# Kernel tuning notes

Hardware: AMD Instinct MI355X
Metric: run time of the kernel (lower is better)

## Reference

```python
import jax, jax.numpy as jnp
import numpy as np

C = 64          # n_channels
NCLS = 10       # output_size
EPS = 1e-5      # GroupNorm eps (torch default)
T0, DT, NSTEPS = 0.0, 0.1, 10  # t0=0, t1=1, dt=0.1 -> 10 fixed RK4 steps


def _gn(x, w, b):
    # GroupNorm(C, C): per-sample, per-channel norm over H,W
    m = x.mean(axis=(2, 3), keepdims=True)
    v = ((x - m) ** 2).mean(axis=(2, 3), keepdims=True)
    return (x - m) * jax.lax.rsqrt(v + EPS) * w[None, :, None, None] + b[None, :, None, None]


def _conv(x, w, b, stride, pad):
    y = jax.lax.conv_general_dilated(x, w, (stride, stride), pad,
                                     dimension_numbers=('NCHW', 'OIHW', 'NCHW'))
    return y + b[None, :, None, None]


def setup_inputs() -> dict:
    key = jax.random.key(0)
    ks = jax.random.split(key, 8)
    rnd = lambda k, shape, s: jax.random.normal(k, shape, jnp.float32) * s
    B = 64
    return dict(
        x=jax.random.normal(ks[0], (B, 1, 130, 130), jnp.float32),
        # downsampler: Conv(1->C,3,1,VALID), GN, ReLU, Conv(C->C,4,2,1), GN, ReLU, Conv(C->C,4,2,1)
        ds_w1=rnd(ks[1], (C, 1, 3, 3), 0.2), ds_b1=jnp.zeros((C,), jnp.float32),
        ds_n1w=jnp.ones((C,), jnp.float32), ds_n1b=jnp.zeros((C,), jnp.float32),
        ds_w2=rnd(ks[2], (C, C, 4, 4), 0.03), ds_b2=jnp.zeros((C,), jnp.float32),
        ds_n2w=jnp.ones((C,), jnp.float32), ds_n2b=jnp.zeros((C,), jnp.float32),
        ds_w3=rnd(ks[3], (C, C, 4, 4), 0.03), ds_b3=jnp.zeros((C,), jnp.float32),
        # ODE RHS: two Conv2d(C+1 -> C, 3, 1, 1) with time channel concat, two GroupNorms
        ode_w1=rnd(ks[4], (C, C + 1, 3, 3), 0.04), ode_b1=jnp.zeros((C,), jnp.float32),
        ode_n1w=jnp.ones((C,), jnp.float32), ode_n1b=jnp.zeros((C,), jnp.float32),
        ode_w2=rnd(ks[5], (C, C + 1, 3, 3), 0.04), ode_b2=jnp.zeros((C,), jnp.float32),
        ode_n2w=jnp.ones((C,), jnp.float32), ode_n2b=jnp.zeros((C,), jnp.float32),
        # classification head: GN, ReLU, GAP, Linear(C -> 10)
        head_nw=jnp.ones((C,), jnp.float32), head_nb=jnp.zeros((C,), jnp.float32),
        head_W=rnd(ks[6], (NCLS, C), 0.1), head_b=jnp.zeros((NCLS,), jnp.float32),
    )


def reference(x, ds_w1, ds_b1, ds_n1w, ds_n1b, ds_w2, ds_b2, ds_n2w, ds_n2b, ds_w3, ds_b3,
              ode_w1, ode_b1, ode_n1w, ode_n1b, ode_w2, ode_b2, ode_n2w, ode_n2b,
              head_nw, head_nb, head_W, head_b):
    P1 = [(1, 1), (1, 1)]
    # ---- downsampler ----
    h = _conv(x, ds_w1, ds_b1, 1, 'VALID')                      # [B,C,128,128]
    h = jax.nn.relu(_gn(h, ds_n1w, ds_n1b))
    h = _conv(h, ds_w2, ds_b2, 2, P1)                           # [B,C,64,64]
    h = jax.nn.relu(_gn(h, ds_n2w, ds_n2b))
    h = _conv(h, ds_w3, ds_b3, 2, P1)                           # [B,C,32,32]

    # ---- ODE layer: fixed-step classic RK4 (tableau_low), 10 steps ----
    def rhs(t, z):
        z = jax.nn.relu(_gn(z, ode_n1w, ode_n1b))
        ts = jnp.full_like(z[:, :1], t)
        z = _conv(jnp.concatenate((ts, z), axis=1), ode_w1, ode_b1, 1, P1)
        z = jax.nn.relu(_gn(z, ode_n2w, ode_n2b))
        ts = jnp.full_like(z[:, :1], t)
        z = _conv(jnp.concatenate((ts, z), axis=1), ode_w2, ode_b2, 1, P1)
        return z

    def step(z, i):
        t = T0 + i * DT
        k1 = rhs(t, z)
        k2 = rhs(t + 0.5 * DT, z + 0.5 * DT * k1)
        k3 = rhs(t + 0.5 * DT, z + 0.5 * DT * k2)
        k4 = rhs(t + DT, z + DT * k3)
        return z + (DT / 6.0) * (k1 + 2.0 * k2 + 2.0 * k3 + k4), None

    h, _ = jax.lax.scan(step, h, jnp.arange(NSTEPS, dtype=jnp.float32))

    # ---- classification head ----
    h = jax.nn.relu(_gn(h, head_nw, head_nb))
    h = h.mean(axis=(2, 3))                                     # AdaptiveAvgPool2d((1,1)) + Flatten
    return h @ head_W.T + head_b                                # [B, 10]
```

## Files before the change

kernel.cpp:

```cpp
#include <hip/hip_runtime.h>

#define BB 64
#define CC 64

typedef __attribute__((ext_vector_type(8))) short short8;
typedef __attribute__((ext_vector_type(4))) short short4v;
typedef __attribute__((ext_vector_type(4))) float f32x4;

__device__ __forceinline__ float bf2f(unsigned short h) {
    unsigned int u = ((unsigned int)h) << 16;
    float f; __builtin_memcpy(&f, &u, 4); return f;
}
__device__ __forceinline__ unsigned short f2bf(float f) {
    unsigned int u; __builtin_memcpy(&u, &f, 4);
    u += 0x7fffu + ((u >> 16) & 1u);
    return (unsigned short)(u >> 16);
}

__global__ __launch_bounds__(256) void conv1stats_kernel(const float* __restrict__ x,
    const float* __restrict__ w1, const float* __restrict__ b1,
    float* __restrict__ ps, float* __restrict__ ps2) {
    __shared__ float sw1[576];
    __shared__ float sb1[64];
    __shared__ float xs[10 * 130];
    int tid = threadIdx.x;
    int qq = blockIdx.x;
    int b = blockIdx.y;
    for (int i = tid; i < 576; i += 256) sw1[i] = w1[i];
    if (tid < 64) sb1[tid] = b1[tid];
    const float* xb = x + (size_t)b * 130 * 130;
    int c = tid >> 2, q = tid & 3;
    float s = 0.f, s2 = 0.f;
    for (int sidx = 0; sidx < 2; sidx++) {
        int row0 = (qq * 2 + sidx) * 8;
        __syncthreads();
        for (int i = tid; i < 1300; i += 256) xs[i] = xb[row0 * 130 + i];
        __syncthreads();
        const float* wc = &sw1[c * 9];
        float bc = sb1[c];
        for (int p = q; p < 1024; p += 4) {
            int y = p >> 7, xx = p & 127;
            float v = bc;
#pragma unroll
            for (int ky = 0; ky < 3; ky++)
#pragma unroll
                for (int kx = 0; kx < 3; kx++)
                    v += xs[(y + ky) * 130 + xx + kx] * wc[ky * 3 + kx];
            s += v; s2 += v * v;
        }
    }
    s  += __shfl_xor(s, 1, 64);  s  += __shfl_xor(s, 2, 64);
    s2 += __shfl_xor(s2, 1, 64); s2 += __shfl_xor(s2, 2, 64);
    if (q == 0) {
        ps [(b * 8 + qq) * 64 + c] = s;
        ps2[(b * 8 + qq) * 64 + c] = s2;
    }
}

__global__ __launch_bounds__(256) void gn1fin_kernel(const float* __restrict__ ps,
    const float* __restrict__ ps2, const float* __restrict__ n1w, const float* __restrict__ n1b,
    float* __restrict__ gn1sc, float* __restrict__ gn1sh) {
    int i = blockIdx.x * 256 + threadIdx.x;
    if (i >= BB * CC) return;
    int c = i & 63, b = i >> 6;
    float s = 0.f, s2 = 0.f;
#pragma unroll
    for (int qq = 0; qq < 8; qq++) {
        s  += ps [(b * 8 + qq) * 64 + c];
        s2 += ps2[(b * 8 + qq) * 64 + c];
    }
    float mean = s / 16384.f;
    float var = s2 / 16384.f - mean * mean;
    float rstd = rsqrtf(var + 1e-5f);
    float sc = rstd * n1w[c];
    gn1sc[i] = sc;
    gn1sh[i] = n1b[c] - mean * sc;
}

__global__ __launch_bounds__(256) void prepack_kernel(const float* __restrict__ w1,
    const float* __restrict__ w2, const float* __restrict__ dw2,
    const float* __restrict__ dw3, unsigned short* __restrict__ Apk,
    float* __restrict__ Stab) {
    int set = blockIdx.y, kc = blockIdx.x, tid = threadIdx.x;
    int nchunk = (set < 2) ? 18 : 32;
    if (kc < nchunk) {
        const float* w = (set == 0) ? w1 : (set == 1) ? w2 : (set == 2) ? dw2 : dw3;
        size_t off = (set == 0) ? 0 : (set == 1) ? 36864 : (set == 2) ? 73728 : 139264;
        for (int e = tid; e < 2048; e += 256) {
            int co = e >> 5, j = e & 31;
            int k = kc * 32 + j;
            int ci = k & 63;
            int tap = k >> 6;
            float val;
            if (set < 2) val = w[(co * 65 + ci + 1) * 9 + tap];
            else         val = w[((co << 6) + ci) * 16 + tap];
            Apk[off + (size_t)kc * 2048 + e] = f2bf(val);
        }
    }
    if (set < 2 && kc == 0) {
        const float* w = set ? w2 : w1;
        for (int t = tid; t < 576; t += 256) {
            int co = t / 9, tap = t % 9;
            Stab[set * 576 + t] = w[(co * 65) * 9 + tap];
        }
    }
}

__global__ __launch_bounds__(256) void ds2mfma_kernel(const float* __restrict__ x,
    const float* __restrict__ w1, const float* __restrict__ b1,
    const float* __restrict__ gn1sc, const float* __restrict__ gn1sh,
    const unsigned short* __restrict__ Apk, const float* __restrict__ bias2,
    unsigned short* __restrict__ h2, float* __restrict__ sums_out) {
    __shared__ unsigned short X[2 * 198 * 64];
    __shared__ float xs[8 * 68];
    __shared__ float sw1[576];
    __shared__ float sb1[64], ssc[64], ssh[64], sb2[64];
    __shared__ float sred[4][64], s2red[4][64];
    int tid = threadIdx.x;
    int b = blockIdx.y;
    int bx = blockIdx.x;
    int xh = bx & 1, sy = bx >> 1;
    int lane = tid & 63, w = tid >> 6;
    int colL = lane & 15, quad = lane >> 4;

    for (int i = tid; i < 576; i += 256) sw1[i] = w1[i];
    if (tid < 64) {
        sb1[tid] = b1[tid];
        ssc[tid] = gn1sc[b * 64 + tid];
        ssh[tid] = gn1sh[b * 64 + tid];
        sb2[tid] = bias2[tid];
    }
    {
        const float* xb = x + (size_t)b * 130 * 130;
        for (int i = tid; i < 544; i += 256) {
            int r = i / 68, cc = i % 68;
            int xr = 4 * sy - 1 + r, xcg = 64 * xh - 1 + cc;
            xs[i] = (xr >= 0 && xr < 130 && xcg >= 0 && xcg < 130) ? xb[xr * 130 + xcg] : 0.f;
        }
    }
    __syncthreads();
    {
        int sub = tid & 7;
        float sbr[8], scr[8], shr[8];
#pragma unroll
        for (int e = 0; e < 8; e++) {
            int c = sub * 8 + e;
            sbr[e] = sb1[c]; scr[e] = ssc[c]; shr[e] = ssh[c];
        }
        for (int i = tid; i < 3168; i += 256) {
            int pidx = i >> 3;
            int ir = pidx / 66, ic = pidx - ir * 66;
            int gy = 4 * sy - 1 + ir, gxg = 64 * xh - 1 + ic;
            short8 o;
            if (gy >= 0 && gy < 128 && gxg >= 0 && gxg < 128) {
#pragma unroll
                for (int e = 0; e < 8; e++) {
                    int c = sub * 8 + e;
                    float v = sbr[e];
#pragma unroll
                    for (int ky = 0; ky < 3; ky++)
#pragma unroll
                        for (int kx = 0; kx < 3; kx++)
                            v += xs[(ir + ky) * 68 + ic + kx] * sw1[c * 9 + ky * 3 + kx];
                    o[e] = (short)f2bf(fmaxf(fmaf(v, scr[e], shr[e]), 0.f));
                }
            } else {
#pragma unroll
                for (int e = 0; e < 8; e++) o[e] = 0;
            }
            int p = ic & 1;
            int psx = ir * 33 + (ic >> 1);
            *(short8*)(X + ((p * 198 + psx) << 6) + ((sub ^ (psx & 7)) << 3)) = o;
        }
    }
    __syncthreads();

    int l = w >> 1, oxb = (w & 1) * 16;
    int oxl = oxb + colL;
    f32x4 acc[4] = {};
    for (int kc = 0; kc < 32; ++kc) {
        int tap = kc >> 1;
        int ky = tap >> 2, kx = tap & 3;
        int chgrp = (kc & 1) * 4 + quad;
        int ir = 2 * l + ky;
        int p = kx & 1;
        int psx = ir * 33 + oxl + (kx >> 1);
        short8 bb = *(const short8*)(X + ((p * 198 + psx) << 6) + ((chgrp ^ (psx & 7)) << 3));
        const unsigned short* ap = Apk + (((kc << 6) + colL) << 5) + (quad << 3);
        short8 a0 = *(const short8*)(ap);
        short8 a1 = *(const short8*)(ap + 512);
        short8 a2 = *(const short8*)(ap + 1024);
        short8 a3 = *(const short8*)(ap + 1536);
        acc[0] = __builtin_amdgcn_mfma_f32_16x16x32_bf16(a0, bb, acc[0], 0, 0, 0);
        acc[1] = __builtin_amdgcn_mfma_f32_16x16x32_bf16(a1, bb, acc[1], 0, 0, 0);
        acc[2] = __builtin_amdgcn_mfma_f32_16x16x32_bf16(a2, bb, acc[2], 0, 0, 0);
        acc[3] = __builtin_amdgcn_mfma_f32_16x16x32_bf16(a3, bb, acc[3], 0, 0, 0);
    }

    float sl[16], s2l[16];
#pragma unroll
    for (int i = 0; i < 16; i++) { sl[i] = 0.f; s2l[i] = 0.f; }
    int oy = 2 * sy + l, oxg = xh * 32 + oxl;
#pragma unroll
    for (int mt = 0; mt < 4; ++mt) {
        int co0 = mt * 16 + quad * 4;
        size_t base = ((size_t)((b * 64 + oy) * 64 + oxg)) * 64 + co0;
        short4v o;
#pragma unroll
        for (int r = 0; r < 4; ++r) {
            unsigned short hh = f2bf(acc[mt][r] + sb2[co0 + r]);
            o[r] = (short)hh;
            float f = bf2f(hh);
            sl[mt * 4 + r] += f; s2l[mt * 4 + r] += f * f;
        }
        *(short4v*)(h2 + base) = o;
    }
#pragma unroll
    for (int idx = 0; idx < 16; ++idx) {
        float s = sl[idx], s2 = s2l[idx];
        s += __shfl_xor(s, 1, 64); s += __shfl_xor(s, 2, 64);
        s += __shfl_xor(s, 4, 64); s += __shfl_xor(s, 8, 64);
        s2 += __shfl_xor(s2, 1, 64); s2 += __shfl_xor(s2, 2, 64);
        s2 += __shfl_xor(s2, 4, 64); s2 += __shfl_xor(s2, 8, 64);
        if (colL == 0) {
            int co = (idx >> 2) * 16 + quad * 4 + (idx & 3);
            sred[w][co] = s; s2red[w][co] = s2;
        }
    }
    __syncthreads();
    if (tid < 64) {
        float s = sred[0][tid] + sred[1][tid] + sred[2][tid] + sred[3][tid];
        float s2 = s2red[0][tid] + s2red[1][tid] + s2red[2][tid] + s2red[3][tid];
        atomicAdd(&sums_out[b * 64 + tid], s);
        atomicAdd(&sums_out[4096 + b * 64 + tid], s2);
    }
}

__global__ __launch_bounds__(256) void ds3mfma_kernel(const unsigned short* __restrict__ h2,
    const float* __restrict__ sums_in, const float* __restrict__ gw, const float* __restrict__ gb,
    const unsigned short* __restrict__ Apk, const float* __restrict__ bias3,
    float* __restrict__ z, unsigned short* __restrict__ zb, float* __restrict__ sums_out) {
    __shared__ unsigned short X[2 * 198 * 64];
    __shared__ float ssc[64], ssh[64], sb3[64];
    __shared__ float sred[4][64], s2red[4][64];
    int tid = threadIdx.x;
    int b = blockIdx.y, sy = blockIdx.x;
    int lane = tid & 63, w = tid >> 6;
    int colL = lane & 15, quad = lane >> 4;

    if (tid < 64) {
        int c = tid;
        float s = sums_in[b * 64 + c];
        float s2 = sums_in[4096 + b * 64 + c];
        float mean = s * (1.f / 4096.f);
        float var = fmaxf(s2 * (1.f / 4096.f) - mean * mean, 0.f);
        float sc = rsqrtf(var + 1e-5f) * gw[c];
        ssc[c] = sc;
        ssh[c] = gb[c] - mean * sc;
        sb3[c] = bias3[c];
    }
    __syncthreads();
    {
        int sub = tid & 7;
        float scr[8], shr[8];
#pragma unroll
        for (int e = 0; e < 8; e++) { scr[e] = ssc[sub * 8 + e]; shr[e] = ssh[sub * 8 + e]; }
        for (int i = tid; i < 3168; i += 256) {
            int pidx = i >> 3;
            int ir = pidx / 66, ic = pidx - ir * 66;
            int gy = 4 * sy - 1 + ir, gx = ic - 1;
            short8 o;
            if (gy >= 0 && gy < 64 && gx >= 0 && gx < 64) {
                short8 d = *(const short8*)(h2 + ((size_t)((b * 64 + gy) * 64 + gx)) * 64 + sub * 8);
#pragma unroll
                for (int e = 0; e < 8; e++) {
                    float f = bf2f((unsigned short)d[e]);
                    o[e] = (short)f2bf(fmaxf(fmaf(f, scr[e], shr[e]), 0.f));
                }
            } else {
#pragma unroll
                for (int e = 0; e < 8; e++) o[e] = 0;
            }
            int p = ic & 1;
            int psx = ir * 33 + (ic >> 1);
            *(short8*)(X + ((p * 198 + psx) << 6) + ((sub ^ (psx & 7)) << 3)) = o;
        }
    }
    __syncthreads();

    int l = w >> 1, oxb = (w & 1) * 16;
    int oxl = oxb + colL;
    f32x4 acc[4] = {};
    for (int kc = 0; kc < 32; ++kc) {
        int tap = kc >> 1;
        int ky = tap >> 2, kx = tap & 3;
        int chgrp = (kc & 1) * 4 + quad;
        int ir = 2 * l + ky;
        int p = kx & 1;
        int psx = ir * 33 + oxl + (kx >> 1);
        short8 bb = *(const short8*)(X + ((p * 198 + psx) << 6) + ((chgrp ^ (psx & 7)) << 3));
        const unsigned short* ap = Apk + (((kc << 6) + colL) << 5) + (quad << 3);
        short8 a0 = *(const short8*)(ap);
        short8 a1 = *(const short8*)(ap + 512);
        short8 a2 = *(const short8*)(ap + 1024);
        short8 a3 = *(const short8*)(ap + 1536);
        acc[0] = __builtin_amdgcn_mfma_f32_16x16x32_bf16(a0, bb, acc[0], 0, 0, 0);
        acc[1] = __builtin_amdgcn_mfma_f32_16x16x32_bf16(a1, bb, acc[1], 0, 0, 0);
        acc[2] = __builtin_amdgcn_mfma_f32_16x16x32_bf16(a2, bb, acc[2], 0, 0, 0);
        acc[3] = __builtin_amdgcn_mfma_f32_16x16x32_bf16(a3, bb, acc[3], 0, 0, 0);
    }

    float sl[16], s2l[16];
#pragma unroll
    for (int i = 0; i < 16; i++) { sl[i] = 0.f; s2l[i] = 0.f; }
    int py = 2 * sy + l;
#pragma unroll
    for (int mt = 0; mt < 4; ++mt) {
        int co0 = mt * 16 + quad * 4;
        size_t base = ((size_t)((b << 10) + py * 32 + oxl)) * 64 + co0;
        f32x4 zv;
        short4v o;
#pragma unroll
        for (int r = 0; r < 4; ++r) {
            float val = acc[mt][r] + sb3[co0 + r];
            zv[r] = val;
            unsigned short hh = f2bf(val);
            o[r] = (short)hh;
            float f = bf2f(hh);
            sl[mt * 4 + r] += f; s2l[mt * 4 + r] += f * f;
        }
        *(f32x4*)(z + base) = zv;
        *(short4v*)(zb + base) = o;
    }
#pragma unroll
    for (int idx = 0; idx < 16; ++idx) {
        float s = sl[idx], s2 = s2l[idx];
        s += __shfl_xor(s, 1, 64); s += __shfl_xor(s, 2, 64);
        s += __shfl_xor(s, 4, 64); s += __shfl_xor(s, 8, 64);
        s2 += __shfl_xor(s2, 1, 64); s2 += __shfl_xor(s2, 2, 64);
        s2 += __shfl_xor(s2, 4, 64); s2 += __shfl_xor(s2, 8, 64);
        if (colL == 0) {
            int co = (idx >> 2) * 16 + quad * 4 + (idx & 3);
            sred[w][co] = s; s2red[w][co] = s2;
        }
    }
    __syncthreads();
    if (tid < 64) {
        float s = sred[0][tid] + sred[1][tid] + sred[2][tid] + sred[3][tid];
        float s2 = s2red[0][tid] + s2red[1][tid] + s2red[2][tid] + s2red[3][tid];
        atomicAdd(&sums_out[b * 64 + tid], s);
        atomicAdd(&sums_out[4096 + b * 64 + tid], s2);
    }
}

#define CONV_LDS_BYTES 124416
__global__ __launch_bounds__(512, 2) void convmfma_kernel(
    const unsigned short* __restrict__ uin, const float* __restrict__ sums_in,
    const float* __restrict__ gw, const float* __restrict__ gb,
    const unsigned short* __restrict__ Apk, const float* __restrict__ stab,
    const float* __restrict__ bias, float t, float aa, int mode,
    float* __restrict__ z, unsigned short* __restrict__ uout,
    float* __restrict__ kacc, float* __restrict__ sums_out)
{
    extern __shared__ unsigned short smem[];
    unsigned short* Aw = smem;
    unsigned short* X  = smem + 36864;
    float* fp    = (float*)(smem + 36864 + 21760);
    float* ssc   = fp;        float* ssh   = fp + 64;
    float* tS    = fp + 128;  float* trow0 = fp + 192;  float* trow2 = fp + 256;
    float* tcol0 = fp + 320;  float* tcol2 = fp + 384;
    float* tc00  = fp + 448;  float* tc02  = fp + 512;
    float* tc20  = fp + 576;  float* tc22  = fp + 640;
    float* sred  = fp + 704;
    float* s2red = fp + 1216;

    int tid = threadIdx.x;
    int b = blockIdx.y, strip = blockIdx.x;
    int y0 = strip * 8;
    int lane = tid & 63, w = tid >> 6;
    int colL = lane & 15, quad = lane >> 4;

    {
        f32x4 zz = 0.f;
        for (int i = tid; i < 2720; i += 512) ((f32x4*)X)[i] = zz;
    }
    for (int i = tid; i < 4608; i += 512) ((f32x4*)Aw)[i] = ((const f32x4*)Apk)[i];

    if (tid < 64) {
        int c = tid;
        float s = sums_in[b * 64 + c];
        float s2 = sums_in[4096 + b * 64 + c];
        float mean = s * (1.f / 1024.f);
        float var = fmaxf(s2 * (1.f / 1024.f) - mean * mean, 0.f);
        float sc = rsqrtf(var + 1e-5f) * gw[c];
        ssc[c] = sc;
        ssh[c] = gb[c] - mean * sc;
    } else if (tid < 128) {
        int co = tid - 64;
        float w0[9];
#pragma unroll
        for (int k = 0; k < 9; k++) w0[k] = stab[co * 9 + k] * t;
        tS[co] = bias[co] + w0[0]+w0[1]+w0[2]+w0[3]+w0[4]+w0[5]+w0[6]+w0[7]+w0[8];
        trow0[co] = w0[0] + w0[1] + w0[2];
        trow2[co] = w0[6] + w0[7] + w0[8];
        tcol0[co] = w0[0] + w0[3] + w0[6];
        tcol2[co] = w0[2] + w0[5] + w0[8];
        tc00[co] = w0[0]; tc02[co] = w0[2]; tc20[co] = w0[6]; tc22[co] = w0[8];
    }
    __syncthreads();

    {
        int sub = tid & 7;
        float scr[8], shr[8];
#pragma unroll
        for (int e = 0; e < 8; e++) { scr[e] = ssc[sub * 8 + e]; shr[e] = ssh[sub * 8 + e]; }
#pragma unroll
        for (int it = 0; it < 5; ++it) {
            int pidx = (tid >> 3) + it * 64;
            int r = pidx >> 5, xc = pidx & 31;
            int gy = y0 - 1 + r;
            if (gy < 0 || gy > 31) continue;
            int gp = (b << 10) + gy * 32 + xc;
            short8 d = *(const short8*)(uin + (size_t)gp * 64 + sub * 8);
            short8 o;
#pragma unroll
            for (int e = 0; e < 8; e++) {
                float f = bf2f((unsigned short)d[e]);
                o[e] = (short)f2bf(fmaxf(fmaf(f, scr[e], shr[e]), 0.f));
            }
            int psx = r * 34 + xc + 1;
            *(short8*)(X + (psx << 6) + ((sub ^ (psx & 7)) << 3)) = o;
        }
    }
    __syncthreads();

    f32x4 acc[4][2] = {};
    for (int kc = 0; kc < 18; ++kc) {
        int tap = kc >> 1;
        int dy = tap / 3, dx = tap % 3;
        int chgrp = (kc & 1) * 4 + quad;
        int ps0 = (w + dy) * 34 + colL + dx;
        int ps1 = ps0 + 16;
        short8 bb0 = *(const short8*)(X + (ps0 << 6) + ((chgrp ^ (ps0 & 7)) << 3));
        short8 bb1 = *(const short8*)(X + (ps1 << 6) + ((chgrp ^ (ps1 & 7)) << 3));
        const unsigned short* ap = Aw + (((kc << 6) + colL) << 5) + (quad << 3);
        short8 a0 = *(const short8*)(ap);
        short8 a1 = *(const short8*)(ap + 512);
        short8 a2 = *(const short8*)(ap + 1024);
        short8 a3 = *(const short8*)(ap + 1536);
        acc[0][0] = __builtin_amdgcn_mfma_f32_16x16x32_bf16(a0, bb0, acc[0][0], 0, 0, 0);
        acc[0][1] = __builtin_amdgcn_mfma_f32_16x16x32_bf16(a0, bb1, acc[0][1], 0, 0, 0);
        acc[1][0] = __builtin_amdgcn_mfma_f32_16x16x32_bf16(a1, bb0, acc[1][0], 0, 0, 0);
        acc[1][1] = __builtin_amdgcn_mfma_f32_16x16x32_bf16(a1, bb1, acc[1][1], 0, 0, 0);
        acc[2][0] = __builtin_amdgcn_mfma_f32_16x16x32_bf16(a2, bb0, acc[2][0], 0, 0, 0);
        acc[2][1] = __builtin_amdgcn_mfma_f32_16x16x32_bf16(a2, bb1, acc[2][1], 0, 0, 0);
        acc[3][0] = __builtin_amdgcn_mfma_f32_16x16x32_bf16(a3, bb0, acc[3][0], 0, 0, 0);
        acc[3][1] = __builtin_amdgcn_mfma_f32_16x16x32_bf16(a3, bb1, acc[3][1], 0, 0, 0);
    }

    float sl[16], s2l[16];
#pragma unroll
    for (int i = 0; i < 16; i++) { sl[i] = 0.f; s2l[i] = 0.f; }
    int py = y0 + w;
    bool by0 = (py == 0), by1 = (py == 31);
#pragma unroll
    for (int nt = 0; nt < 2; ++nt) {
        int px = nt * 16 + colL;
        bool bx0 = (px == 0), bx1 = (px == 31);
#pragma unroll
        for (int mt = 0; mt < 4; ++mt) {
            int co0 = mt * 16 + quad * 4;
            float vout[4];
#pragma unroll
            for (int r = 0; r < 4; ++r) {
                int co = co0 + r;
                float val = acc[mt][nt][r] + tS[co];
                if (by0) { val -= trow0[co]; if (bx0) val += tc00[co]; if (bx1) val += tc02[co]; }
                if (by1) { val -= trow2[co]; if (bx0) val += tc20[co]; if (bx1) val += tc22[co]; }
                if (bx0) val -= tcol0[co];
                if (bx1) val -= tcol2[co];
                vout[r] = val;
            }
            size_t base = ((size_t)((b << 10) + py * 32 + px)) * 64 + co0;
            if (mode == 3) {
                short4v o;
#pragma unroll
                for (int r = 0; r < 4; ++r) {
                    unsigned short hh = f2bf(vout[r]);
                    o[r] = (short)hh;
                    float f = bf2f(hh);
                    sl[mt * 4 + r] += f; s2l[mt * 4 + r] += f * f;
                }
                *(short4v*)(uout + base) = o;
            } else if (mode == 2) {
                f32x4 kv = *(const f32x4*)(kacc + base);
                f32x4 zv = *(const f32x4*)(z + base);
                short4v o;
#pragma unroll
                for (int r = 0; r < 4; ++r) {
                    float zn = zv[r] + aa * (kv[r] + vout[r]);
                    zv[r] = zn;
                    unsigned short hh = f2bf(zn);
                    o[r] = (short)hh;
                    float f = bf2f(hh);
                    sl[mt * 4 + r] += f; s2l[mt * 4 + r] += f * f;
                }
                *(f32x4*)(z + base) = zv;
                *(short4v*)(uout + base) = o;
            } else {
                f32x4 zv = *(const f32x4*)(z + base);
                f32x4 kv;
                if (mode == 1) {
                    kv = *(const f32x4*)(kacc + base);
#pragma unroll
                    for (int r = 0; r < 4; ++r) kv[r] += 2.f * vout[r];
                } else {
#pragma unroll
                    for (int r = 0; r < 4; ++r) kv[r] = vout[r];
                }
                *(f32x4*)(kacc + base) = kv;
                short4v o;
#pragma unroll
                for (int r = 0; r < 4; ++r) {
                    unsigned short hh = f2bf(zv[r] + aa * vout[r]);
                    o[r] = (short)hh;
                    float f = bf2f(hh);
                    sl[mt * 4 + r] += f; s2l[mt * 4 + r] += f * f;
                }
                *(short4v*)(uout + base) = o;
            }
        }
    }
#pragma unroll
    for (int idx = 0; idx < 16; ++idx) {
        float s = sl[idx], s2 = s2l[idx];
        s += __shfl_xor(s, 1, 64); s += __shfl_xor(s, 2, 64);
        s += __shfl_xor(s, 4, 64); s += __shfl_xor(s, 8, 64);
        s2 += __shfl_xor(s2, 1, 64); s2 += __shfl_xor(s2, 2, 64);
        s2 += __shfl_xor(s2, 4, 64); s2 += __shfl_xor(s2, 8, 64);
        if (colL == 0) {
            int co = (idx >> 2) * 16 + quad * 4 + (idx & 3);
            sred[w * 64 + co] = s; s2red[w * 64 + co] = s2;
        }
    }
    __syncthreads();
    if (tid < 64) {
        float s = 0.f, s2 = 0.f;
#pragma unroll
        for (int i = 0; i < 8; i++) { s += sred[i * 64 + tid]; s2 += s2red[i * 64 + tid]; }
        atomicAdd(&sums_out[b * 64 + tid], s);
        atomicAdd(&sums_out[4096 + b * 64 + tid], s2);
    }
}

__global__ __launch_bounds__(256) void headgap_kernel(const float* __restrict__ z,
    const float* __restrict__ w, const float* __restrict__ b, float* __restrict__ pooled) {
    __shared__ float r1[4][64], r2[4][64];
    __shared__ float scs[64], shs[64];
    int bq = blockIdx.x, tid = threadIdx.x;
    int c = tid & 63, g = tid >> 6;
    float s = 0.f, s2 = 0.f;
    for (int p = g; p < 1024; p += 4) {
        float v = z[((size_t)((bq << 10) + p)) * 64 + c];
        s += v; s2 += v * v;
    }
    r1[g][c] = s; r2[g][c] = s2;
    __syncthreads();
    if (tid < 64) {
        float ts = r1[0][tid] + r1[1][tid] + r1[2][tid] + r1[3][tid];
        float ts2 = r2[0][tid] + r2[1][tid] + r2[2][tid] + r2[3][tid];
        float mean = ts / 1024.f;
        float var = fmaxf(ts2 / 1024.f - mean * mean, 0.f);
        float sc = rsqrtf(var + 1e-5f) * w[tid];
        scs[tid] = sc;
        shs[tid] = b[tid] - mean * sc;
    }
    __syncthreads();
    float sc = scs[c], sh = shs[c];
    float r = 0.f;
    for (int p = g; p < 1024; p += 4)
        r += fmaxf(fmaf(z[((size_t)((bq << 10) + p)) * 64 + c], sc, sh), 0.f);
    r1[g][c] = r;
    __syncthreads();
    if (tid < 64)
        pooled[bq * 64 + tid] = (r1[0][tid] + r1[1][tid] + r1[2][tid] + r1[3][tid]) / 1024.f;
}

__global__ __launch_bounds__(256) void headfc_kernel(const float* __restrict__ pooled,
    const float* __restrict__ W, const float* __restrict__ bias, float* __restrict__ out) {
    int i = blockIdx.x * 256 + threadIdx.x;
    if (i < 640) {
        int b = i / 10, j = i % 10;
        float a = bias[j];
        const float* p = pooled + b * 64;
        const float* wj = W + j * 64;
#pragma unroll 8
        for (int c = 0; c < 64; c++) a += p[c] * wj[c];
        out[i] = a;
    }
}

extern "C" void kernel_launch(void* const* d_in, const int* in_sizes, int n_in,
                              void* d_out, int out_size, void* d_ws, size_t ws_size,
                              hipStream_t stream) {
    const float* x      = (const float*)d_in[0];
    const float* ds_w1  = (const float*)d_in[1];
    const float* ds_b1  = (const float*)d_in[2];
    const float* ds_n1w = (const float*)d_in[3];
    const float* ds_n1b = (const float*)d_in[4];
    const float* ds_w2  = (const float*)d_in[5];
    const float* ds_b2  = (const float*)d_in[6];
    const float* ds_n2w = (const float*)d_in[7];
    const float* ds_n2b = (const float*)d_in[8];
    const float* ds_w3  = (const float*)d_in[9];
    const float* ds_b3  = (const float*)d_in[10];
    const float* ode_w1 = (const float*)d_in[11];
    const float* ode_b1 = (const float*)d_in[12];
    const float* ode_n1w= (const float*)d_in[13];
    const float* ode_n1b= (const float*)d_in[14];
    const float* ode_w2 = (const float*)d_in[15];
    const float* ode_b2 = (const float*)d_in[16];
    const float* ode_n2w= (const float*)d_in[17];
    const float* ode_n2b= (const float*)d_in[18];
    const float* head_nw= (const float*)d_in[19];
    const float* head_nb= (const float*)d_in[20];
    const float* head_W = (const float*)d_in[21];
    const float* head_b = (const float*)d_in[22];

    const size_t NZ = (size_t)BB * CC * 32 * 32;
    float* ws = (float*)d_ws;
    float*          z     = ws;
    unsigned short* zb    = (unsigned short*)(ws + NZ);
    unsigned short* u     = (unsigned short*)(ws + 3 * NZ / 2);
    unsigned short* v     = (unsigned short*)(ws + 2 * NZ);
    float*          kacc  = ws + 5 * NZ / 2;
    unsigned short* h2    = u;
    float*          apf   = ws + 7 * NZ / 2;
    unsigned short* Apk   = (unsigned short*)apf;
    float*          Stab  = apf + 102400;
    float*          sums  = Stab + 1152;
    float*          ps    = sums + 82 * 8192;
    float*          ps2   = ps + 32768;
    float*          gn1sc = ps2 + 32768;
    float*          gn1sh = gn1sc + 4096;
    float*          pooled= gn1sh + 4096;

    auto SUM = [&](int s) { return sums + (size_t)s * 8192; };
    auto SV = [&](int i, int j) { return 1 + i * 7 + j; };
    auto SU = [&](int i, int j) { return 1 + i * 7 + 4 + j; };
    auto ZS = [&](int i) { return 71 + i; };
    const int H2S = 81;

    hipFuncSetAttribute(reinterpret_cast<const void*>(convmfma_kernel),
                        hipFuncAttributeMaxDynamicSharedMemorySize, CONV_LDS_BYTES);

    hipMemsetAsync(sums, 0, 82 * 8192 * sizeof(float), stream);
    prepack_kernel<<<dim3(32, 4), 256, 0, stream>>>(ode_w1, ode_w2, ds_w2, ds_w3, Apk, Stab);

    conv1stats_kernel<<<dim3(8, BB), 256, 0, stream>>>(x, ds_w1, ds_b1, ps, ps2);
    gn1fin_kernel<<<16, 256, 0, stream>>>(ps, ps2, ds_n1w, ds_n1b, gn1sc, gn1sh);
    ds2mfma_kernel<<<dim3(64, BB), 256, 0, stream>>>(x, ds_w1, ds_b1, gn1sc, gn1sh,
        Apk + 73728, ds_b2, h2, SUM(H2S));
    ds3mfma_kernel<<<dim3(16, BB), 256, 0, stream>>>(h2, SUM(H2S), ds_n2w, ds_n2b,
        Apk + 139264, ds_b3, z, zb, SUM(0));

    const unsigned short* AP1 = Apk;
    const unsigned short* AP2 = Apk + 36864;
    const float* ST1 = Stab;
    const float* ST2 = Stab + 576;
    const float c6 = 0.1f / 6.0f;
    dim3 cgrid(4, BB);
    for (int i = 0; i < 10; i++) {
        float t0 = 0.1f * (float)i;
        int zslot = (i == 0) ? 0 : ZS(i - 1);
        convmfma_kernel<<<cgrid, 512, CONV_LDS_BYTES, stream>>>(zb, SUM(zslot), ode_n1w, ode_n1b,
            AP1, ST1, ode_b1, t0, 0.f, 3, z, v, kacc, SUM(SV(i, 0)));
        convmfma_kernel<<<cgrid, 512, CONV_LDS_BYTES, stream>>>(v, SUM(SV(i, 0)), ode_n2w, ode_n2b,
            AP2, ST2, ode_b2, t0, 0.05f, 0, z, u, kacc, SUM(SU(i, 0)));
        convmfma_kernel<<<cgrid, 512, CONV_LDS_BYTES, stream>>>(u, SUM(SU(i, 0)), ode_n1w, ode_n1b,
            AP1, ST1, ode_b1, t0 + 0.05f, 0.f, 3, z, v, kacc, SUM(SV(i, 1)));
        convmfma_kernel<<<cgrid, 512, CONV_LDS_BYTES, stream>>>(v, SUM(SV(i, 1)), ode_n2w, ode_n2b,
            AP2, ST2, ode_b2, t0 + 0.05f, 0.05f, 1, z, u, kacc, SUM(SU(i, 1)));
        convmfma_kernel<<<cgrid, 512, CONV_LDS_BYTES, stream>>>(u, SUM(SU(i, 1)), ode_n1w, ode_n1b,
            AP1, ST1, ode_b1, t0 + 0.05f, 0.f, 3, z, v, kacc, SUM(SV(i, 2)));
        convmfma_kernel<<<cgrid, 512, CONV_LDS_BYTES, stream>>>(v, SUM(SV(i, 2)), ode_n2w, ode_n2b,
            AP2, ST2, ode_b2, t0 + 0.05f, 0.1f, 1, z, u, kacc, SUM(SU(i, 2)));
        convmfma_kernel<<<cgrid, 512, CONV_LDS_BYTES, stream>>>(u, SUM(SU(i, 2)), ode_n1w, ode_n1b,
            AP1, ST1, ode_b1, t0 + 0.1f, 0.f, 3, z, v, kacc, SUM(SV(i, 3)));
        convmfma_kernel<<<cgrid, 512, CONV_LDS_BYTES, stream>>>(v, SUM(SV(i, 3)), ode_n2w, ode_n2b,
            AP2, ST2, ode_b2, t0 + 0.1f, c6, 2, z, zb, kacc, SUM(ZS(i)));
    }

    headgap_kernel<<<BB, 256, 0, stream>>>(z, head_nw, head_nb, pooled);
    headfc_kernel<<<3, 256, 0, stream>>>(pooled, head_W, head_b, (float*)d_out);
}
```

Before: 2.250 ms.

## Replace atomic GroupNorm stats with per-block partial slots; store RK4 accumulator in bf16

Each block now writes its per-channel sum and sum-of-squares partials to its own slot, and the consumer kernel adds up the partials. This replaces global atomicAdd and removes the memset of the sums buffer. The RK4 k-accumulator is stored in bf16 instead of fp32, and the intermediate stages read z from the bf16 copy instead of fp32 z. Together these cut global memory traffic in each conv launch, at the cost of extra rounding in the k accumulation and the stage inputs.

```diff
diff --git a/kernel.cpp b/kernel.cpp
--- a/kernel.cpp
+++ b/kernel.cpp
@@ -231,8 +231,8 @@
     if (tid < 64) {
         float s = sred[0][tid] + sred[1][tid] + sred[2][tid] + sred[3][tid];
         float s2 = s2red[0][tid] + s2red[1][tid] + s2red[2][tid] + s2red[3][tid];
-        atomicAdd(&sums_out[b * 64 + tid], s);
-        atomicAdd(&sums_out[4096 + b * 64 + tid], s2);
+        sums_out[(size_t)bx * 8192 + b * 64 + tid] = s;
+        sums_out[(size_t)bx * 8192 + 4096 + b * 64 + tid] = s2;
     }
 }
 
@@ -250,8 +250,9 @@
 
     if (tid < 64) {
         int c = tid;
-        float s = sums_in[b * 64 + c];
-        float s2 = sums_in[4096 + b * 64 + c];
+        float s = 0.f, s2 = 0.f;
+        const float* sp = sums_in + b * 64 + c;
+        for (int i = 0; i < 64; i++) { s += sp[(size_t)i * 8192]; s2 += sp[(size_t)i * 8192 + 4096]; }
         float mean = s * (1.f / 4096.f);
         float var = fmaxf(s2 * (1.f / 4096.f) - mean * mean, 0.f);
         float sc = rsqrtf(var + 1e-5f) * gw[c];
@@ -348,19 +349,20 @@
     if (tid < 64) {
         float s = sred[0][tid] + sred[1][tid] + sred[2][tid] + sred[3][tid];
         float s2 = s2red[0][tid] + s2red[1][tid] + s2red[2][tid] + s2red[3][tid];
-        atomicAdd(&sums_out[b * 64 + tid], s);
-        atomicAdd(&sums_out[4096 + b * 64 + tid], s2);
+        sums_out[(size_t)sy * 8192 + b * 64 + tid] = s;
+        sums_out[(size_t)sy * 8192 + 4096 + b * 64 + tid] = s2;
     }
 }
 
 #define CONV_LDS_BYTES 124416
 __global__ __launch_bounds__(512, 2) void convmfma_kernel(
-    const unsigned short* __restrict__ uin, const float* __restrict__ sums_in,
+    const unsigned short* __restrict__ uin, const float* __restrict__ sums_in, int nsub,
     const float* __restrict__ gw, const float* __restrict__ gb,
     const unsigned short* __restrict__ Apk, const float* __restrict__ stab,
     const float* __restrict__ bias, float t, float aa, int mode,
-    float* __restrict__ z, unsigned short* __restrict__ uout,
-    float* __restrict__ kacc, float* __restrict__ sums_out)
+    float* __restrict__ z, const unsigned short* __restrict__ zbin,
+    unsigned short* __restrict__ uout, unsigned short* __restrict__ kacc,
+    float* __restrict__ sums_out)
 {
     extern __shared__ unsigned short smem[];
     unsigned short* Aw = smem;
@@ -388,8 +390,9 @@
 
     if (tid < 64) {
         int c = tid;
-        float s = sums_in[b * 64 + c];
-        float s2 = sums_in[4096 + b * 64 + c];
+        float s = 0.f, s2 = 0.f;
+        const float* sp = sums_in + b * 64 + c;
+        for (int i = 0; i < nsub; i++) { s += sp[(size_t)i * 8192]; s2 += sp[(size_t)i * 8192 + 4096]; }
         float mean = s * (1.f / 1024.f);
         float var = fmaxf(s2 * (1.f / 1024.f) - mean * mean, 0.f);
         float sc = rsqrtf(var + 1e-5f) * gw[c];
@@ -493,12 +496,12 @@
                 }
                 *(short4v*)(uout + base) = o;
             } else if (mode == 2) {
-                f32x4 kv = *(const f32x4*)(kacc + base);
+                short4v kv = *(const short4v*)(kacc + base);
                 f32x4 zv = *(const f32x4*)(z + base);
                 short4v o;
 #pragma unroll
                 for (int r = 0; r < 4; ++r) {
-                    float zn = zv[r] + aa * (kv[r] + vout[r]);
+                    float zn = zv[r] + aa * (bf2f((unsigned short)kv[r]) + vout[r]);
                     zv[r] = zn;
                     unsigned short hh = f2bf(zn);
                     o[r] = (short)hh;
@@ -508,21 +511,22 @@
                 *(f32x4*)(z + base) = zv;
                 *(short4v*)(uout + base) = o;
             } else {
-                f32x4 zv = *(const f32x4*)(z + base);
-                f32x4 kv;
+                short4v zs = *(const short4v*)(zbin + base);
+                short4v ko, o;
                 if (mode == 1) {
-                    kv = *(const f32x4*)(kacc + base);
-#pragma unroll
-                    for (int r = 0; r < 4; ++r) kv[r] += 2.f * vout[r];
+                    short4v kv = *(const short4v*)(kacc + base);
+#pragma unroll
+                    for (int r = 0; r < 4; ++r)
+                        ko[r] = (short)f2bf(bf2f((unsigned short)kv[r]) + 2.f * vout[r]);
                 } else {
 #pragma unroll
-                    for (int r = 0; r < 4; ++r) kv[r] = vout[r];
+                    for (int r = 0; r < 4; ++r) ko[r] = (short)f2bf(vout[r]);
                 }
-                *(f32x4*)(kacc + base) = kv;
-                short4v o;
+                *(short4v*)(kacc + base) = ko;
 #pragma unroll
                 for (int r = 0; r < 4; ++r) {
-                    unsigned short hh = f2bf(zv[r] + aa * vout[r]);
+                    float zf = bf2f((unsigned short)zs[r]);
+                    unsigned short hh = f2bf(zf + aa * vout[r]);
                     o[r] = (short)hh;
                     float f = bf2f(hh);
                     sl[mt * 4 + r] += f; s2l[mt * 4 + r] += f * f;
@@ -548,8 +552,8 @@
         float s = 0.f, s2 = 0.f;
 #pragma unroll
         for (int i = 0; i < 8; i++) { s += sred[i * 64 + tid]; s2 += s2red[i * 64 + tid]; }
-        atomicAdd(&sums_out[b * 64 + tid], s);
-        atomicAdd(&sums_out[4096 + b * 64 + tid], s2);
+        sums_out[(size_t)strip * 8192 + b * 64 + tid] = s;
+        sums_out[(size_t)strip * 8192 + 4096 + b * 64 + tid] = s2;
     }
 }
 
@@ -633,36 +637,33 @@
     unsigned short* zb    = (unsigned short*)(ws + NZ);
     unsigned short* u     = (unsigned short*)(ws + 3 * NZ / 2);
     unsigned short* v     = (unsigned short*)(ws + 2 * NZ);
-    float*          kacc  = ws + 5 * NZ / 2;
+    unsigned short* kacc  = (unsigned short*)(ws + 5 * NZ / 2);
     unsigned short* h2    = u;
     float*          apf   = ws + 7 * NZ / 2;
     unsigned short* Apk   = (unsigned short*)apf;
     float*          Stab  = apf + 102400;
-    float*          sums  = Stab + 1152;
-    float*          ps    = sums + 82 * 8192;
+    float*          ds2s  = Stab + 1152;
+    float*          zsum  = ds2s + (size_t)64 * 8192;
+    float*          osl   = zsum + (size_t)16 * 8192;
+    float*          ps    = osl + (size_t)80 * 32768;
     float*          ps2   = ps + 32768;
     float*          gn1sc = ps2 + 32768;
     float*          gn1sh = gn1sc + 4096;
     float*          pooled= gn1sh + 4096;
 
-    auto SUM = [&](int s) { return sums + (size_t)s * 8192; };
-    auto SV = [&](int i, int j) { return 1 + i * 7 + j; };
-    auto SU = [&](int i, int j) { return 1 + i * 7 + 4 + j; };
-    auto ZS = [&](int i) { return 71 + i; };
-    const int H2S = 81;
+    auto OSL = [&](int j) { return osl + (size_t)j * 32768; };
 
     hipFuncSetAttribute(reinterpret_cast<const void*>(convmfma_kernel),
                         hipFuncAttributeMaxDynamicSharedMemorySize, CONV_LDS_BYTES);
 
-    hipMemsetAsync(sums, 0, 82 * 8192 * sizeof(float), stream);
     prepack_kernel<<<dim3(32, 4), 256, 0, stream>>>(ode_w1, ode_w2, ds_w2, ds_w3, Apk, Stab);
 
     conv1stats_kernel<<<dim3(8, BB), 256, 0, stream>>>(x, ds_w1, ds_b1, ps, ps2);
     gn1fin_kernel<<<16, 256, 0, stream>>>(ps, ps2, ds_n1w, ds_n1b, gn1sc, gn1sh);
     ds2mfma_kernel<<<dim3(64, BB), 256, 0, stream>>>(x, ds_w1, ds_b1, gn1sc, gn1sh,
-        Apk + 73728, ds_b2, h2, SUM(H2S));
-    ds3mfma_kernel<<<dim3(16, BB), 256, 0, stream>>>(h2, SUM(H2S), ds_n2w, ds_n2b,
-        Apk + 139264, ds_b3, z, zb, SUM(0));
+        Apk + 73728, ds_b2, h2, ds2s);
+    ds3mfma_kernel<<<dim3(16, BB), 256, 0, stream>>>(h2, ds2s, ds_n2w, ds_n2b,
+        Apk + 139264, ds_b3, z, zb, zsum);
 
     const unsigned short* AP1 = Apk;
     const unsigned short* AP2 = Apk + 36864;
@@ -672,23 +673,25 @@
     dim3 cgrid(4, BB);
     for (int i = 0; i < 10; i++) {
         float t0 = 0.1f * (float)i;
-        int zslot = (i == 0) ? 0 : ZS(i - 1);
-        convmfma_kernel<<<cgrid, 512, CONV_LDS_BYTES, stream>>>(zb, SUM(zslot), ode_n1w, ode_n1b,
-            AP1, ST1, ode_b1, t0, 0.f, 3, z, v, kacc, SUM(SV(i, 0)));
-        convmfma_kernel<<<cgrid, 512, CONV_LDS_BYTES, stream>>>(v, SUM(SV(i, 0)), ode_n2w, ode_n2b,
-            AP2, ST2, ode_b2, t0, 0.05f, 0, z, u, kacc, SUM(SU(i, 0)));
-        convmfma_kernel<<<cgrid, 512, CONV_LDS_BYTES, stream>>>(u, SUM(SU(i, 0)), ode_n1w, ode_n1b,
-            AP1, ST1, ode_b1, t0 + 0.05f, 0.f, 3, z, v, kacc, SUM(SV(i, 1)));
-        convmfma_kernel<<<cgrid, 512, CONV_LDS_BYTES, stream>>>(v, SUM(SV(i, 1)), ode_n2w, ode_n2b,
-            AP2, ST2, ode_b2, t0 + 0.05f, 0.05f, 1, z, u, kacc, SUM(SU(i, 1)));
-        convmfma_kernel<<<cgrid, 512, CONV_LDS_BYTES, stream>>>(u, SUM(SU(i, 1)), ode_n1w, ode_n1b,
-            AP1, ST1, ode_b1, t0 + 0.05f, 0.f, 3, z, v, kacc, SUM(SV(i, 2)));
-        convmfma_kernel<<<cgrid, 512, CONV_LDS_BYTES, stream>>>(v, SUM(SV(i, 2)), ode_n2w, ode_n2b,
-            AP2, ST2, ode_b2, t0 + 0.05f, 0.1f, 1, z, u, kacc, SUM(SU(i, 2)));
-        convmfma_kernel<<<cgrid, 512, CONV_LDS_BYTES, stream>>>(u, SUM(SU(i, 2)), ode_n1w, ode_n1b,
-            AP1, ST1, ode_b1, t0 + 0.1f, 0.f, 3, z, v, kacc, SUM(SV(i, 3)));
-        convmfma_kernel<<<cgrid, 512, CONV_LDS_BYTES, stream>>>(v, SUM(SV(i, 3)), ode_n2w, ode_n2b,
-            AP2, ST2, ode_b2, t0 + 0.1f, c6, 2, z, zb, kacc, SUM(ZS(i)));
+        int j = 8 * i;
+        const float* s0 = (i == 0) ? zsum : OSL(j - 1);
+        int n0 = (i == 0) ? 16 : 4;
+        convmfma_kernel<<<cgrid, 512, CONV_LDS_BYTES, stream>>>(zb, s0, n0, ode_n1w, ode_n1b,
+            AP1, ST1, ode_b1, t0, 0.f, 3, z, zb, v, kacc, OSL(j));
+        convmfma_kernel<<<cgrid, 512, CONV_LDS_BYTES, stream>>>(v, OSL(j), 4, ode_n2w, ode_n2b,
+            AP2, ST2, ode_b2, t0, 0.05f, 0, z, zb, u, kacc, OSL(j + 1));
+        convmfma_kernel<<<cgrid, 512, CONV_LDS_BYTES, stream>>>(u, OSL(j + 1), 4, ode_n1w, ode_n1b,
+            AP1, ST1, ode_b1, t0 + 0.05f, 0.f, 3, z, zb, v, kacc, OSL(j + 2));
+        convmfma_kernel<<<cgrid, 512, CONV_LDS_BYTES, stream>>>(v, OSL(j + 2), 4, ode_n2w, ode_n2b,
+            AP2, ST2, ode_b2, t0 + 0.05f, 0.05f, 1, z, zb, u, kacc, OSL(j + 3));
+        convmfma_kernel<<<cgrid, 512, CONV_LDS_BYTES, stream>>>(u, OSL(j + 3), 4, ode_n1w, ode_n1b,
+            AP1, ST1, ode_b1, t0 + 0.05f, 0.f, 3, z, zb, v, kacc, OSL(j + 4));
+        convmfma_kernel<<<cgrid, 512, CONV_LDS_BYTES, stream>>>(v, OSL(j + 4), 4, ode_n2w, ode_n2b,
+            AP2, ST2, ode_b2, t0 + 0.05f, 0.1f, 1, z, zb, u, kacc, OSL(j + 5));
+        convmfma_kernel<<<cgrid, 512, CONV_LDS_BYTES, stream>>>(u, OSL(j + 5), 4, ode_n1w, ode_n1b,
+            AP1, ST1, ode_b1, t0 + 0.1f, 0.f, 3, z, zb, v, kacc, OSL(j + 6));
+        convmfma_kernel<<<cgrid, 512, CONV_LDS_BYTES, stream>>>(v, OSL(j + 6), 4, ode_n2w, ode_n2b,
+            AP2, ST2, ode_b2, t0 + 0.1f, c6, 2, z, zb, zb, kacc, OSL(j + 7));
     }
 
     headgap_kernel<<<BB, 256, 0, stream>>>(z, head_nw, head_nb, pooled);
```

Result: no change. 2.242 ms (-0.4%).
